# Performance work log

Measured on AMD Instinct MI355X. Metric: run time of the kernel, lower is better.

The kernel has to match this reference:

```python
import jax, jax.numpy as jnp
import numpy as np

N_NODES = 50000
D = 100          # hidden_size == out_size
STEP = 1
B, N, L = 512, 64, 64
STDV = 1.0 / np.sqrt(D)


def _uniform(key, shape):
    return jax.random.uniform(key, shape, jnp.float32, -STDV, STDV)


def setup_inputs() -> dict:
    key = jax.random.key(0)
    ks = jax.random.split(key, 16)
    inp = {
        'adj_in': jax.random.uniform(ks[0], (B, N, N), jnp.float32),
        'adj_out': jax.random.uniform(ks[1], (B, N, N), jnp.float32),
        'item': jax.random.randint(ks[2], (B, N), 0, N_NODES, jnp.int32),
        'alias': jax.random.randint(ks[3], (B, L), 0, N, jnp.int32),
        'mask': jnp.ones((B, L), jnp.float32),
        'tar': jax.random.randint(ks[4], (B,), 0, N_NODES - 1, jnp.int32) + 1,
        # learned parameters
        'embedding': _uniform(ks[5], (N_NODES, D)),
        'W_in': _uniform(ks[6], (D, D)),
        'b_in': _uniform(ks[7], (D,)),
        'W_out': _uniform(ks[8], (D, D)),
        'b_out': _uniform(ks[9], (D,)),
        'gate_kernel': _uniform(ks[10], (3 * D, 2 * D)),
        'gate_bias': jnp.ones((2 * D,), jnp.float32),
        'cand_kernel': _uniform(ks[11], (3 * D, D)),
        'cand_bias': jnp.zeros((D,), jnp.float32),
        'nasr_w1': _uniform(ks[12], (D, D)),
        'nasr_w2': _uniform(ks[13], (D, D)),
        'nasr_v': _uniform(ks[14], (1, D)),
        'nasr_b': jnp.zeros((D,), jnp.float32),
    }
    return inp


def _ggnn(embedding, item, adj_in, adj_out, W_in, b_in, W_out, b_out,
          gate_kernel, gate_bias, cand_kernel, cand_bias):
    fin = embedding[item]                                 # [B, N, D]
    for _ in range(STEP):
        fi = jnp.einsum('bnd,de->bne', fin, W_in) + b_in   # [B, N, D]
        fo = jnp.einsum('bnd,de->bne', fin, W_out) + b_out
        av = jnp.concatenate([jnp.matmul(adj_in, fi), jnp.matmul(adj_out, fo)], axis=-1)  # [B, N, 2D]
        x = av.reshape(-1, 2 * D)
        h = fin.reshape(-1, D)
        # TF GRUCell math
        gates = jax.nn.sigmoid(jnp.concatenate([x, h], -1) @ gate_kernel + gate_bias)
        r, u = jnp.split(gates, 2, axis=-1)
        c = jnp.tanh(jnp.concatenate([x, r * h], -1) @ cand_kernel + cand_bias)
        fin = (u * h + (1.0 - u) * c).reshape(fin.shape)
    return fin


def _forward(adj_in, adj_out, mask, embedding, W_in, b_in, W_out, b_out,
             gate_kernel, gate_bias, cand_kernel, cand_bias,
             nasr_w1, nasr_w2, nasr_v, nasr_b, item, alias, tar):
    re = _ggnn(embedding, item, adj_in, adj_out, W_in, b_in, W_out, b_out,
               gate_kernel, gate_bias, cand_kernel, cand_bias)   # [B, N, D]
    bsz = re.shape[0]
    rm = jnp.sum(mask, axis=1).astype(jnp.int32)                 # [B]
    rows = jnp.arange(bsz)
    last_id = alias[rows, rm - 1]                                # [B]
    last_h = re[rows, last_id]                                   # [B, D]
    seq_h = jnp.take_along_axis(re, alias[..., None], axis=1)    # [B, L, D]
    last = last_h @ nasr_w1                                      # [B, D]
    seq = jnp.einsum('bld,de->ble', seq_h, nasr_w2)              # [B, L, D]
    m = jax.nn.sigmoid(last[:, None, :] + seq + nasr_b)          # [B, L, D]
    coef = (m @ nasr_v[0]) * mask                                # [B, L]
    ma = jnp.sum(coef[..., None] * seq_h, axis=1)                # [B, D]
    logits = ma @ embedding[1:].T                                # [B, n_nodes-1]
    labels = tar - 1
    logp = jax.nn.log_softmax(logits, axis=-1)
    loss = -jnp.mean(logp[rows, labels])
    return loss, logits


def reference(adj_in, adj_out, item, alias, mask, tar, embedding,
              W_in, b_in, W_out, b_out, gate_kernel, gate_bias,
              cand_kernel, cand_bias, nasr_w1, nasr_w2, nasr_v, nasr_b):
    return _forward(adj_in, adj_out, mask, embedding, W_in, b_in, W_out, b_out,
                    gate_kernel, gate_bias, cand_kernel, cand_bias,
                    nasr_w1, nasr_w2, nasr_v, nasr_b, item, alias, tar)
```

## Files before the change

### kernel.cpp

```cpp
#include <hip/hip_runtime.h>
#include <math.h>

#define BB    512
#define NNODE 64
#define LLEN  64
#define DD    100
#define NNODES 50000
#define NM1   49999
#define KP    128
#define KAV   224
#define KTOT  352
#define NCB   391
#define SHIFT 20.0f

typedef __attribute__((ext_vector_type(8))) short short8;
typedef __attribute__((ext_vector_type(4))) short short4_t;
typedef __attribute__((ext_vector_type(4))) float f32x4;
typedef unsigned short ushort_t;

__device__ __forceinline__ float sigm(float x) { return 1.0f / (1.0f + __expf(-x)); }
__device__ __forceinline__ float mytanh(float x) {
  x = fminf(15.0f, fmaxf(-15.0f, x));
  float e = __expf(-2.0f * x);
  return (1.0f - e) / (1.0f + e);
}
__device__ __forceinline__ float f4c(const float4& v, int k) { return ((const float*)&v)[k]; }
__device__ __forceinline__ ushort_t f2bf(float f) {
  union { float f; unsigned u; } v; v.f = f;
  unsigned r = v.u + 0x7FFF + ((v.u >> 16) & 1);
  return (ushort_t)(r >> 16);
}
__device__ __forceinline__ float bf2f(ushort_t s) {
  union { unsigned u; float f; } v; v.u = ((unsigned)s) << 16;
  return v.f;
}
__device__ __forceinline__ short8 cvt8(const float* __restrict__ p) {
  float4 v0 = *(const float4*)p, v1 = *(const float4*)(p + 4);
  short8 r;
  r[0] = (short)f2bf(v0.x); r[1] = (short)f2bf(v0.y);
  r[2] = (short)f2bf(v0.z); r[3] = (short)f2bf(v0.w);
  r[4] = (short)f2bf(v1.x); r[5] = (short)f2bf(v1.y);
  r[6] = (short)f2bf(v1.z); r[7] = (short)f2bf(v1.w);
  return r;
}

__global__ __launch_bounds__(256) void k_cvt_all(
    const float* __restrict__ emb,
    const float* __restrict__ Wi, const float* __restrict__ Wo,
    const float* __restrict__ gk, const float* __restrict__ ck,
    ushort_t* __restrict__ eb2, ushort_t* __restrict__ WioT,
    ushort_t* __restrict__ gkT, ushort_t* __restrict__ ckT,
    float* __restrict__ sumrow)
{
  const int bid = blockIdx.x, t = threadIdx.x;
  if (bid < 782) {
    const int tid = bid * 256 + t;
    const int r = tid >> 2;
    if (r >= NNODES) return;
    const int c0 = (tid & 3) * 32;
#pragma unroll
    for (int c4 = c0; c4 < c0 + 32; c4 += 4) {
      short4_t o = {0, 0, 0, 0};
      if (c4 < DD) {
        float4 v = *(const float4*)(emb + (size_t)r * DD + c4);
        o.x = (short)f2bf(f4c(v, 0)); o.y = (short)f2bf(f4c(v, 1));
        o.z = (short)f2bf(f4c(v, 2)); o.w = (short)f2bf(f4c(v, 3));
      }
      *(short4_t*)(eb2 + (size_t)r * KP + c4) = o;
    }
    return;
  }
  if (bid == 1643) {
    sumrow[t] = 0.0f;
    sumrow[t + 256] = 0.0f;
    return;
  }
  const int rem = bid - 782;
  const int y = rem / 287;
  const int idx = (rem - y * 287) * 256 + t;
  if (y == 0) {
    if (idx >= 208 * 128) return;
    int n = idx >> 7, k = idx & 127;
    float v = 0.0f;
    if (k < DD) {
      if (n < 100) v = Wi[k * DD + n];
      else if (n < 200) v = Wo[k * DD + (n - 100)];
    }
    WioT[idx] = f2bf(v);
  } else if (y == 1) {
    if (idx >= 208 * KTOT) return;
    int n = idx / KTOT, k = idx - n * KTOT;
    float v = 0.0f;
    if (n < 200) {
      if (k < KAV) { if (k < 200) v = gk[k * 200 + n]; }
      else { int kk = k - KAV; if (kk < 100) v = gk[(200 + kk) * 200 + n]; }
    }
    gkT[idx] = f2bf(v);
  } else {
    if (idx >= 112 * KTOT) return;
    int n = idx / KTOT, k = idx - n * KTOT;
    float v = 0.0f;
    if (n < 100) {
      if (k < KAV) { if (k < 200) v = ck[k * DD + n]; }
      else { int kk = k - KAV; if (kk < 100) v = ck[(200 + kk) * DD + n]; }
    }
    ckT[idx] = f2bf(v);
  }
}

__global__ __launch_bounds__(512) void k_fused(
    const ushort_t* __restrict__ eb2, const int* __restrict__ item,
    const ushort_t* __restrict__ WioT,
    const float* __restrict__ bi, const float* __restrict__ bo,
    const float* __restrict__ adj_in, const float* __restrict__ adj_out,
    const ushort_t* __restrict__ gkT, const float* __restrict__ gb,
    const ushort_t* __restrict__ ckT, const float* __restrict__ cbs,
    const int* __restrict__ alias_, const float* __restrict__ mask,
    const float* __restrict__ w1, const float* __restrict__ w2,
    const float* __restrict__ nv, const float* __restrict__ nb,
    ushort_t* __restrict__ mab)
{
  __shared__ __align__(16) char pool[80320];
  ushort_t (*s_f)[112][72] = (ushort_t (*)[112][72])(pool);
  ushort_t (*s_rh)[136]    = (ushort_t (*)[136])(pool);
  ushort_t (*s_ub)[104]    = (ushort_t (*)[104])(pool + 17408);
  float    (*s_m)[104]     = (float (*)[104])(pool);
  ushort_t (*s_av)[232]    = (ushort_t (*)[232])(pool + 32256);
  float    (*s_fin)[104]   = (float (*)[104])(pool + 32256);
  ushort_t (*s_h)[136]     = (ushort_t (*)[136])(pool + 61952);
  float* s_last   = (float*)(pool + 79360);
  float* s_coef   = (float*)(pool + 79776);
  int*   s_idx    = (int*)(pool + 80032);
  int*   s_lastid = (int*)(pool + 80288);

  const int t = threadIdx.x;
  const int w8 = t >> 6, lane = t & 63;
  const int rw = w8 & 3, ch = w8 >> 2;
  const int n16 = lane & 15, quad = lane >> 4;
  const int b = blockIdx.x;

  {
    const int row = t >> 3, seg = t & 7;
    const ushort_t* hsrc = eb2 + (size_t)item[b * 64 + row] * KP + seg * 16;
    *(short8*)&s_h[row][seg * 16]     = *(const short8*)(hsrc);
    *(short8*)&s_h[row][seg * 16 + 8] = *(const short8*)(hsrc + 8);
  }
  if (t >= 64 && t < 128) {
    const int r2 = t - 64;
#pragma unroll
    for (int c = 200; c < 224; ++c) s_av[r2][c] = 0;
  }
  for (int idx = t; idx < 2 * 12 * 64; idx += 512) {
    int which = idx / 768, rem = idx - which * 768;
    s_f[which][100 + rem / 64][rem & 63] = 0;
  }
  __syncthreads();

  short8 af[4];
#pragma unroll
  for (int ks = 0; ks < 4; ++ks)
    af[ks] = *(const short8*)&s_h[rw * 16 + n16][quad * 8 + ks * 32];

  {
    const int node0 = rw * 16 + quad * 4;
    const int s0 = ch ? 7 : 0, s1 = ch ? 13 : 7;
    for (int sub = s0; sub < s1; ++sub) {
      const ushort_t* brow = WioT + (size_t)(sub * 16 + n16) * KP + quad * 8;
      f32x4 acc = {0.0f, 0.0f, 0.0f, 0.0f};
#pragma unroll
      for (int ks = 0; ks < 4; ++ks)
        acc = __builtin_amdgcn_mfma_f32_16x16x32_bf16(af[ks], *(const short8*)(brow + ks * 32), acc, 0, 0, 0);
      const int col = sub * 16 + n16;
      if (col < 200) {
        const float bias = (col < 100) ? bi[col] : bo[col - 100];
        short4_t st;
#pragma unroll
        for (int r = 0; r < 4; ++r) ((ushort_t*)&st)[r] = f2bf(acc[r] + bias);
        const int which = (col < 100) ? 0 : 1;
        const int c = (col < 100) ? col : col - 100;
        *(short4_t*)&s_f[which][c][node0] = st;
      }
    }
  }
  __syncthreads();

  {
    const float* aX = (ch ? adj_out : adj_in)
                      + ((size_t)b * 64 + rw * 16 + n16) * 64 + quad * 8;
    short8 afX[2];
    afX[0] = cvt8(aX); afX[1] = cvt8(aX + 32);
    for (int sub = 0; sub < 7; ++sub) {
      const int col = sub * 16 + n16;
      const ushort_t* bX = &s_f[ch][col][quad * 8];
      f32x4 acc = {0.0f, 0.0f, 0.0f, 0.0f};
#pragma unroll
      for (int ks = 0; ks < 2; ++ks)
        acc = __builtin_amdgcn_mfma_f32_16x16x32_bf16(afX[ks], *(const short8*)(bX + ks * 32), acc, 0, 0, 0);
      if (col < 100) {
#pragma unroll
        for (int r = 0; r < 4; ++r)
          s_av[rw * 16 + quad * 4 + r][ch * 100 + col] = f2bf(acc[r]);
      }
    }
  }
  __syncthreads();

  if (t < 64) {
#pragma unroll
    for (int c = 100; c < 128; ++c) s_rh[t][c] = 0;
  }
  short8 afa[7];
#pragma unroll
  for (int ks = 0; ks < 7; ++ks)
    afa[ks] = *(const short8*)&s_av[rw * 16 + n16][quad * 8 + ks * 32];

  {
    const int s0 = ch ? 7 : 0, s1 = ch ? 13 : 7;
    for (int sub = s0; sub < s1; ++sub) {
      const ushort_t* brow = gkT + (size_t)(sub * 16 + n16) * KTOT + quad * 8;
      f32x4 acc = {0.0f, 0.0f, 0.0f, 0.0f};
#pragma unroll
      for (int ks = 0; ks < 7; ++ks)
        acc = __builtin_amdgcn_mfma_f32_16x16x32_bf16(afa[ks], *(const short8*)(brow + ks * 32), acc, 0, 0, 0);
#pragma unroll
      for (int ks = 0; ks < 4; ++ks)
        acc = __builtin_amdgcn_mfma_f32_16x16x32_bf16(af[ks], *(const short8*)(brow + KAV + ks * 32), acc, 0, 0, 0);
      const int col = sub * 16 + n16;
      if (col < 200) {
        const float bias = gb[col];
#pragma unroll
        for (int r = 0; r < 4; ++r) {
          const int row = rw * 16 + quad * 4 + r;
          const float g = sigm(acc[r] + bias);
          if (col < 100) s_rh[row][col] = f2bf(g * bf2f(s_h[row][col]));
          else           s_ub[row][col - 100] = f2bf(g);
        }
      }
    }
  }
  __syncthreads();

  short8 afr[4];
#pragma unroll
  for (int ks = 0; ks < 4; ++ks)
    afr[ks] = *(const short8*)&s_rh[rw * 16 + n16][quad * 8 + ks * 32];

  {
    const int s0 = ch ? 4 : 0, s1 = ch ? 7 : 4;
    for (int sub = s0; sub < s1; ++sub) {
      const ushort_t* brow = ckT + (size_t)(sub * 16 + n16) * KTOT + quad * 8;
      f32x4 acc = {0.0f, 0.0f, 0.0f, 0.0f};
#pragma unroll
      for (int ks = 0; ks < 7; ++ks)
        acc = __builtin_amdgcn_mfma_f32_16x16x32_bf16(afa[ks], *(const short8*)(brow + ks * 32), acc, 0, 0, 0);
#pragma unroll
      for (int ks = 0; ks < 4; ++ks)
        acc = __builtin_amdgcn_mfma_f32_16x16x32_bf16(afr[ks], *(const short8*)(brow + KAV + ks * 32), acc, 0, 0, 0);
      const int col = sub * 16 + n16;
      if (col < 100) {
        const float bias = cbs[col];
#pragma unroll
        for (int r = 0; r < 4; ++r) {
          const int row = rw * 16 + quad * 4 + r;
          const float c_ = mytanh(acc[r] + bias);
          const float u = bf2f(s_ub[row][col]);
          const float hv = bf2f(s_h[row][col]);
          s_fin[row][col] = u * hv + (1.0f - u) * c_;
        }
      }
    }
  }
  __syncthreads();

  if (t < 64) {
    float v = mask[b * LLEN + t];
    v += __shfl_xor(v, 1, 64);  v += __shfl_xor(v, 2, 64);
    v += __shfl_xor(v, 4, 64);  v += __shfl_xor(v, 8, 64);
    v += __shfl_xor(v, 16, 64); v += __shfl_xor(v, 32, 64);
    if (t == 0) {
      int rm = (int)(v + 0.5f);
      *s_lastid = alias_[b * LLEN + rm - 1];
    }
  } else if (t < 128) {
    s_idx[t - 64] = alias_[b * LLEN + (t - 64)];
  }
  __syncthreads();

  if (t < DD) {
    const float* lh = s_fin[*s_lastid];
    float acc = 0.0f;
#pragma unroll 4
    for (int k = 0; k < DD; ++k) acc += lh[k] * w1[k * DD + t];
    s_last[t] = acc;
  }
  __syncthreads();

  {
    const int tx = t & 31, ty = t >> 5, cb4 = tx * 4;
    if (cb4 < DD) {
      float acc[4][4] = {};
      const float* frs[4] = { s_fin[s_idx[ty * 4 + 0]], s_fin[s_idx[ty * 4 + 1]],
                              s_fin[s_idx[ty * 4 + 2]], s_fin[s_idx[ty * 4 + 3]] };
      for (int k4 = 0; k4 < 25; ++k4) {
        float4 bv[4];
#pragma unroll
        for (int kk = 0; kk < 4; ++kk)
          bv[kk] = *(const float4*)(w2 + (size_t)(k4 * 4 + kk) * DD + cb4);
#pragma unroll
        for (int i = 0; i < 4; ++i) {
          float4 a = *(const float4*)(frs[i] + k4 * 4);
#pragma unroll
          for (int kk = 0; kk < 4; ++kk) {
            float av_ = f4c(a, kk);
#pragma unroll
            for (int j = 0; j < 4; ++j) acc[i][j] += av_ * f4c(bv[kk], j);
          }
        }
      }
#pragma unroll
      for (int i = 0; i < 4; ++i) {
        const int l = ty * 4 + i;
#pragma unroll
        for (int j = 0; j < 4; ++j) {
          const int e = cb4 + j;
          s_m[l][e] = sigm(acc[i][j] + s_last[e] + nb[e]);
        }
      }
    }
  }
  __syncthreads();

  if (t < LLEN) {
    float acc = 0.0f;
#pragma unroll 4
    for (int e = 0; e < DD; ++e) acc += s_m[t][e] * nv[e];
    s_coef[t] = acc * mask[b * LLEN + t];
  }
  __syncthreads();

  if (t < DD) {
    float acc = 0.0f;
#pragma unroll 4
    for (int l = 0; l < LLEN; ++l) acc += s_coef[l] * s_fin[s_idx[l]][t];
    mab[(size_t)b * KP + t] = f2bf(acc);
  } else if (t < KP) {
    mab[(size_t)b * KP + t] = 0;
  }
}

__global__ __launch_bounds__(256) void k_logits_mfma(
    const ushort_t* __restrict__ eb2, const ushort_t* __restrict__ mab,
    float* __restrict__ out, float* __restrict__ sumrow)
{
  __shared__ float s_o[16][512];
  const int t = threadIdx.x;
  const int wave = t >> 6, lane = t & 63;
  const int n16 = lane & 15, quad = lane >> 4;
  const int bid = blockIdx.x;
  const int xcd = bid & 7;
  const int j = bid >> 3;
  const int grpl = j >> 5;
  const int lgmax = (xcd < 2) ? 13 : 12;
  if (grpl >= lgmax) return;
  const int stripe = j & 31;
  const int cg = ((xcd < 2) ? xcd * 13 : 26 + (xcd - 2) * 12) + grpl;
  const int m0 = stripe * 16;
  const int cblk = cg * 4 + wave;

  short8 afr[4];
  const ushort_t* abase = mab + (size_t)(m0 + n16) * KP + quad * 8;
#pragma unroll
  for (int ks = 0; ks < 4; ++ks) afr[ks] = *(const short8*)(abase + ks * 32);

  float s[4] = {0.0f, 0.0f, 0.0f, 0.0f};
  if (cblk < NCB) {
#pragma unroll
    for (int sub = 0; sub < 8; ++sub) {
      const int c = cblk * 128 + sub * 16 + n16;
      const ushort_t* bbase = eb2 + (size_t)((c < NM1) ? (c + 1) : 0) * KP + quad * 8;
      f32x4 acc = {0.0f, 0.0f, 0.0f, 0.0f};
#pragma unroll
      for (int ks = 0; ks < 4; ++ks) {
        short8 bfr = *(const short8*)(bbase + ks * 32);
        acc = __builtin_amdgcn_mfma_f32_16x16x32_bf16(afr[ks], bfr, acc, 0, 0, 0);
      }
#pragma unroll
      for (int r = 0; r < 4; ++r) {
        s_o[quad * 4 + r][wave * 128 + sub * 16 + n16] = acc[r];
        if (c < NM1) s[r] += __expf(acc[r] - SHIFT);
      }
    }
  }
  __syncthreads();

  float* lgp = out + 1;
  const int half = t >> 7, tc = t & 127;
#pragma unroll
  for (int it = 0; it < 8; ++it) {
    const int row = it * 2 + half;
    const size_t gr = m0 + row;
    f32x4 v = *(const f32x4*)&s_o[row][tc * 4];
    const int c0 = cg * 512 + tc * 4;
    if (c0 + 3 < NM1) {
      __builtin_nontemporal_store(v, (f32x4*)(lgp + gr * NM1 + c0));
    } else {
#pragma unroll
      for (int e = 0; e < 4; ++e)
        if (c0 + e < NM1)
          __builtin_nontemporal_store(v[e], lgp + gr * NM1 + c0 + e);
    }
  }

  if (cblk < NCB) {
    const int row0 = m0 + quad * 4;
#pragma unroll
    for (int r = 0; r < 4; ++r) {
      float x = s[r];
      x += __shfl_xor(x, 1, 64);
      x += __shfl_xor(x, 2, 64);
      x += __shfl_xor(x, 4, 64);
      x += __shfl_xor(x, 8, 64);
      if (n16 == 0) atomicAdd(&sumrow[row0 + r], x);
    }
  }
}

__global__ __launch_bounds__(512) void k_lse_loss(
    const float* __restrict__ sumrow, float* __restrict__ out,
    const int* __restrict__ tar)
{
  const int r = threadIdx.x;
  __shared__ float red[8];
  const float* lg = out + 1;
  const int label = tar[r] - 1;
  float rt = lg[(size_t)r * NM1 + label] - (logf(sumrow[r]) + SHIFT);
  for (int m = 1; m < 64; m <<= 1) rt += __shfl_xor(rt, m, 64);
  if ((r & 63) == 0) red[r >> 6] = rt;
  __syncthreads();
  if (r == 0) {
    float tot = 0.0f;
#pragma unroll
    for (int i = 0; i < 8; ++i) tot += red[i];
    out[0] = -tot / (float)BB;
  }
}

extern "C" void kernel_launch(void* const* d_in, const int* in_sizes, int n_in,
                              void* d_out, int out_size, void* d_ws, size_t ws_size,
                              hipStream_t stream)
{
  (void)in_sizes; (void)n_in; (void)out_size; (void)ws_size;
  const float* adj_in  = (const float*)d_in[0];
  const float* adj_out = (const float*)d_in[1];
  const int*   item    = (const int*)d_in[2];
  const int*   alias_  = (const int*)d_in[3];
  const float* mask    = (const float*)d_in[4];
  const int*   tar     = (const int*)d_in[5];
  const float* emb     = (const float*)d_in[6];
  const float* W_in    = (const float*)d_in[7];
  const float* b_in    = (const float*)d_in[8];
  const float* W_out   = (const float*)d_in[9];
  const float* b_out   = (const float*)d_in[10];
  const float* gk      = (const float*)d_in[11];
  const float* gb      = (const float*)d_in[12];
  const float* ck      = (const float*)d_in[13];
  const float* cbs     = (const float*)d_in[14];
  const float* w1      = (const float*)d_in[15];
  const float* w2      = (const float*)d_in[16];
  const float* nv      = (const float*)d_in[17];
  const float* nb      = (const float*)d_in[18];
  float* out = (float*)d_out;

  ushort_t* usw = (ushort_t*)d_ws;
  ushort_t* eb2  = usw;
  ushort_t* WioT = usw + 13740032;
  ushort_t* gkT  = usw + 13766656;
  ushort_t* ckT  = usw + 13839872;
  ushort_t* mab  = usw + 13879296;
  float* fpool   = (float*)(usw + 13944832);
  float* sumrow  = fpool + 3276800;

  k_cvt_all <<<dim3(1644), 256, 0, stream>>>(emb, W_in, W_out, gk, ck,
                                             eb2, WioT, gkT, ckT, sumrow);
  k_fused   <<<dim3(512), 512, 0, stream>>>(eb2, item, WioT, b_in, b_out,
                                            adj_in, adj_out, gkT, gb, ckT, cbs,
                                            alias_, mask, w1, w2, nv, nb, mab);
  k_logits_mfma<<<dim3(3328), 256, 0, stream>>>(eb2, mab, out, sumrow);
  k_lse_loss<<<dim3(1), 512, 0, stream>>>(sumrow, out, tar);
}
```

Measured before the change: 312.4 us.

## Drop bf16 embedding pre-conversion; convert fp32 embedding rows on the fly in consumers

The embedding table is no longer converted into a padded bf16 copy by a separate pass. The fused GGNN kernel and the logits MFMA kernel now read fp32 embedding rows directly and convert them to bf16 in registers, and the weight-conversion kernel shrinks to a 2D grid that handles only the small weight matrices and the sumrow reset. This removes a full read of the fp32 table plus a write of the padded bf16 copy. In exchange, the logits kernel reads twice as many bytes per embedding row, and its reads of 100-float rows are less aligned than the 128-wide padded layout.

```diff
diff --git a/kernel.cpp b/kernel.cpp
--- a/kernel.cpp
+++ b/kernel.cpp
@@ -44,41 +44,21 @@
   return r;
 }
 
-__global__ __launch_bounds__(256) void k_cvt_all(
-    const float* __restrict__ emb,
+__global__ __launch_bounds__(256) void k_cvt_w(
     const float* __restrict__ Wi, const float* __restrict__ Wo,
     const float* __restrict__ gk, const float* __restrict__ ck,
-    ushort_t* __restrict__ eb2, ushort_t* __restrict__ WioT,
-    ushort_t* __restrict__ gkT, ushort_t* __restrict__ ckT,
-    float* __restrict__ sumrow)
+    ushort_t* __restrict__ WioT, ushort_t* __restrict__ gkT,
+    ushort_t* __restrict__ ckT, float* __restrict__ sumrow)
 {
-  const int bid = blockIdx.x, t = threadIdx.x;
-  if (bid < 782) {
-    const int tid = bid * 256 + t;
-    const int r = tid >> 2;
-    if (r >= NNODES) return;
-    const int c0 = (tid & 3) * 32;
-#pragma unroll
-    for (int c4 = c0; c4 < c0 + 32; c4 += 4) {
-      short4_t o = {0, 0, 0, 0};
-      if (c4 < DD) {
-        float4 v = *(const float4*)(emb + (size_t)r * DD + c4);
-        o.x = (short)f2bf(f4c(v, 0)); o.y = (short)f2bf(f4c(v, 1));
-        o.z = (short)f2bf(f4c(v, 2)); o.w = (short)f2bf(f4c(v, 3));
-      }
-      *(short4_t*)(eb2 + (size_t)r * KP + c4) = o;
-    }
-    return;
-  }
-  if (bid == 1643) {
-    sumrow[t] = 0.0f;
-    sumrow[t + 256] = 0.0f;
-    return;
-  }
-  const int rem = bid - 782;
-  const int y = rem / 287;
-  const int idx = (rem - y * 287) * 256 + t;
+  const int t = threadIdx.x;
+  const int y = blockIdx.y;
+  const int idx = blockIdx.x * 256 + t;
   if (y == 0) {
+    if (blockIdx.x == 286) {
+      sumrow[t] = 0.0f;
+      sumrow[t + 256] = 0.0f;
+      return;
+    }
     if (idx >= 208 * 128) return;
     int n = idx >> 7, k = idx & 127;
     float v = 0.0f;
@@ -109,7 +89,7 @@
 }
 
 __global__ __launch_bounds__(512) void k_fused(
-    const ushort_t* __restrict__ eb2, const int* __restrict__ item,
+    const float* __restrict__ emb, const int* __restrict__ item,
     const ushort_t* __restrict__ WioT,
     const float* __restrict__ bi, const float* __restrict__ bo,
     const float* __restrict__ adj_in, const float* __restrict__ adj_out,
@@ -141,9 +121,19 @@
 
   {
     const int row = t >> 3, seg = t & 7;
-    const ushort_t* hsrc = eb2 + (size_t)item[b * 64 + row] * KP + seg * 16;
-    *(short8*)&s_h[row][seg * 16]     = *(const short8*)(hsrc);
-    *(short8*)&s_h[row][seg * 16 + 8] = *(const short8*)(hsrc + 8);
+    const float* hsrc = emb + (size_t)item[b * 64 + row] * DD + seg * 16;
+    short8 o0 = {0, 0, 0, 0, 0, 0, 0, 0};
+    short8 o1 = {0, 0, 0, 0, 0, 0, 0, 0};
+    if (seg < 6) {
+      o0 = cvt8(hsrc);
+      o1 = cvt8(hsrc + 8);
+    } else if (seg == 6) {
+      float4 v = *(const float4*)(hsrc);
+      o0[0] = (short)f2bf(v.x); o0[1] = (short)f2bf(v.y);
+      o0[2] = (short)f2bf(v.z); o0[3] = (short)f2bf(v.w);
+    }
+    *(short8*)&s_h[row][seg * 16]     = o0;
+    *(short8*)&s_h[row][seg * 16 + 8] = o1;
   }
   if (t >= 64 && t < 128) {
     const int r2 = t - 64;
@@ -349,7 +339,7 @@
 }
 
 __global__ __launch_bounds__(256) void k_logits_mfma(
-    const ushort_t* __restrict__ eb2, const ushort_t* __restrict__ mab,
+    const float* __restrict__ emb, const ushort_t* __restrict__ mab,
     float* __restrict__ out, float* __restrict__ sumrow)
 {
   __shared__ float s_o[16][512];
@@ -377,13 +367,21 @@
 #pragma unroll
     for (int sub = 0; sub < 8; ++sub) {
       const int c = cblk * 128 + sub * 16 + n16;
-      const ushort_t* bbase = eb2 + (size_t)((c < NM1) ? (c + 1) : 0) * KP + quad * 8;
+      const float* browf = emb + (size_t)((c < NM1) ? (c + 1) : 0) * DD;
+      short8 b0 = cvt8(browf + quad * 8);
+      short8 b1 = cvt8(browf + quad * 8 + 32);
+      short8 b2 = cvt8(browf + quad * 8 + 64);
+      short8 b3 = {0, 0, 0, 0, 0, 0, 0, 0};
+      if (quad == 0) {
+        float4 v = *(const float4*)(browf + 96);
+        b3[0] = (short)f2bf(v.x); b3[1] = (short)f2bf(v.y);
+        b3[2] = (short)f2bf(v.z); b3[3] = (short)f2bf(v.w);
+      }
       f32x4 acc = {0.0f, 0.0f, 0.0f, 0.0f};
-#pragma unroll
-      for (int ks = 0; ks < 4; ++ks) {
-        short8 bfr = *(const short8*)(bbase + ks * 32);
-        acc = __builtin_amdgcn_mfma_f32_16x16x32_bf16(afr[ks], bfr, acc, 0, 0, 0);
-      }
+      acc = __builtin_amdgcn_mfma_f32_16x16x32_bf16(afr[0], b0, acc, 0, 0, 0);
+      acc = __builtin_amdgcn_mfma_f32_16x16x32_bf16(afr[1], b1, acc, 0, 0, 0);
+      acc = __builtin_amdgcn_mfma_f32_16x16x32_bf16(afr[2], b2, acc, 0, 0, 0);
+      acc = __builtin_amdgcn_mfma_f32_16x16x32_bf16(afr[3], b3, acc, 0, 0, 0);
 #pragma unroll
       for (int r = 0; r < 4; ++r) {
         s_o[quad * 4 + r][wave * 128 + sub * 16 + n16] = acc[r];
@@ -472,7 +470,6 @@
   float* out = (float*)d_out;
 
   ushort_t* usw = (ushort_t*)d_ws;
-  ushort_t* eb2  = usw;
   ushort_t* WioT = usw + 13740032;
   ushort_t* gkT  = usw + 13766656;
   ushort_t* ckT  = usw + 13839872;
@@ -480,11 +477,11 @@
   float* fpool   = (float*)(usw + 13944832);
   float* sumrow  = fpool + 3276800;
 
-  k_cvt_all <<<dim3(1644), 256, 0, stream>>>(emb, W_in, W_out, gk, ck,
-                                             eb2, WioT, gkT, ckT, sumrow);
-  k_fused   <<<dim3(512), 512, 0, stream>>>(eb2, item, WioT, b_in, b_out,
+  k_cvt_w   <<<dim3(287, 3), 256, 0, stream>>>(W_in, W_out, gk, ck,
+                                               WioT, gkT, ckT, sumrow);
+  k_fused   <<<dim3(512), 512, 0, stream>>>(emb, item, WioT, b_in, b_out,
                                             adj_in, adj_out, gkT, gb, ckT, cbs,
                                             alias_, mask, w1, w2, nv, nb, mab);
-  k_logits_mfma<<<dim3(3328), 256, 0, stream>>>(eb2, mab, out, sumrow);
+  k_logits_mfma<<<dim3(3328), 256, 0, stream>>>(emb, mab, out, sumrow);
   k_lse_loss<<<dim3(1), 512, 0, stream>>>(sumrow, out, tar);
 }
```

Result: faster. 295.5 us (median of 2 runs) (-5.4%).
